# Kernel tuning notes

Hardware: AMD Instinct MI355X
Metric: run time of the kernel (lower is better)

The kernel has to match this reference:

```python
import jax, jax.numpy as jnp
import numpy as np

RES_SAMPLE = [-0.4, -0.3, -0.2, -0.1, 0.0, 0.1, 0.2, 0.3, 0.4]
GROUP_NUM = 8


def setup_inputs() -> dict:
    key = jax.random.key(0)
    k1, k2, k3, k4 = jax.random.split(key, 4)
    B, C, H, W = 4, 32, 256, 256
    return {
        "feat_ref": jax.random.normal(k1, (B, C, H, W), dtype=jnp.float32),
        "feat_ls": jax.random.normal(k2, (B, C, H, W), dtype=jnp.float32),
        "feat_rs": jax.random.normal(k3, (B, C, H, W), dtype=jnp.float32),
        "disp_init": jax.random.uniform(k4, (B, 1, H, W), dtype=jnp.float32),
    }


def _bilerp_chw(feat, x, y):
    """Bilinear sample feat [C,H,W] at pixel coords x,y [H,W], zeros padding
    (matches F.grid_sample(mode='bilinear', padding_mode='zeros'))."""
    C, H, W = feat.shape
    x0 = jnp.floor(x); y0 = jnp.floor(y)
    x1 = x0 + 1.0;     y1 = y0 + 1.0
    wx1 = x - x0; wx0 = 1.0 - wx1
    wy1 = y - y0; wy0 = 1.0 - wy1

    def gather(yi, xi):
        valid = (yi >= 0) & (yi <= H - 1) & (xi >= 0) & (xi <= W - 1)
        yc = jnp.clip(yi, 0, H - 1).astype(jnp.int32)
        xc = jnp.clip(xi, 0, W - 1).astype(jnp.int32)
        return feat[:, yc, xc] * valid.astype(feat.dtype)  # [C,H,W]

    return (gather(y0, x0) * (wy0 * wx0)
            + gather(y0, x1) * (wy0 * wx1)
            + gather(y1, x0) * (wy1 * wx0)
            + gather(y1, x1) * (wy1 * wx1))


def _warp_all_disp(feat, disp, x_dist):
    """feat [B,C,H,W], disp [B,D,H,W] -> warped [B,C,D,H,W] (y_dist=0)."""
    B, C, H, W = feat.shape
    xx = jnp.arange(W, dtype=feat.dtype)[None, :] * jnp.ones((H, 1), feat.dtype)  # [H,W]
    yy = jnp.arange(H, dtype=feat.dtype)[:, None] * jnp.ones((1, W), feat.dtype)  # [H,W]

    def per_b(feat_b, disp_b):  # feat_b [C,H,W], disp_b [D,H,W]
        x = xx[None] + x_dist * disp_b                      # [D,H,W]
        y = jnp.broadcast_to(yy, x.shape)                   # [D,H,W]
        return jax.vmap(lambda xs, ys: _bilerp_chw(feat_b, xs, ys))(x, y)  # [D,C,H,W]

    out = jax.vmap(per_b)(feat, disp)                       # [B,D,C,H,W]
    return out.transpose(0, 2, 1, 3, 4)                     # [B,C,D,H,W]


def reference(feat_ref, feat_ls, feat_rs, disp_init):
    B, C, H, W = feat_ref.shape
    res = jnp.asarray(RES_SAMPLE, dtype=feat_ref.dtype)     # [D]
    D = res.shape[0]
    disp = disp_init[:, 0][:, None] + res[None, :, None, None]  # [B,D,H,W]

    warp_left = _warp_all_disp(feat_ls, disp, 1.0)          # [B,C,D,H,W]
    warp_right = _warp_all_disp(feat_rs, disp, -1.0)        # [B,C,D,H,W]
    fr = feat_ref[:, :, None]                                # [B,C,1,H,W]

    mu = (warp_left + warp_right + fr) / 3.0
    var = ((warp_left - mu) ** 2 + (warp_right - mu) ** 2 + (fr - mu) ** 2) / 3.0

    cpg = C // GROUP_NUM
    cost = var.reshape(B, GROUP_NUM, cpg, D, H, W).mean(axis=2)  # [B,G,D,H,W]
    return cost
```

## Files before the change

kernel.cpp:

```cpp
#include <hip/hip_runtime.h>


#define B_ 4
#define C_ 32
#define H_ 256
#define W_ 256
#define D_ 9
#define G_ 8
#define CPG 4
#define HW_ (H_ * W_)
#define SW_ 260

typedef float v2f __attribute__((ext_vector_type(2)));

static __device__ __forceinline__ v2f sp(float x) {
    v2f r; r.x = x; r.y = x; return r;
}

__global__ __launch_bounds__(256) void cost_volume_kernel(
    const float* __restrict__ fref,
    const float* __restrict__ fls,
    const float* __restrict__ frs,
    const float* __restrict__ disp0,
    float* __restrict__ out)
{
    const float kRes[D_] = {-0.4f, -0.3f, -0.2f, -0.1f, 0.0f,
                             0.1f,  0.2f,  0.3f,  0.4f};

    __shared__ float sL[CPG][SW_];
    __shared__ float sR[CPG][SW_];

    const int bid = blockIdx.x;
    const int g = bid & (G_ - 1);
    const int t = bid >> 3;
    const int h = t & (H_ - 1);
    const int b = t >> 8;
    const int w = threadIdx.x;

    const float dbase = disp0[(unsigned)((b * H_ + h) * W_ + w)];

    const unsigned rowbase = (unsigned)(((b * C_ + g * CPG) * HW_) + h * W_);
    const float* __restrict__ refrow = fref + rowbase;
    const float* __restrict__ lsrow  = fls  + rowbase;
    const float* __restrict__ rsrow  = frs  + rowbase;

    {
        const int x = w - 2;
        const bool v = (unsigned)x < (unsigned)W_;
        #pragma unroll
        for (int cc = 0; cc < CPG; ++cc) {
            sL[cc][w] = v ? lsrow[cc * HW_ + x] : 0.0f;
            sR[cc][w] = v ? rsrow[cc * HW_ + x] : 0.0f;
        }
        if (w < SW_ - W_) {
            const int x2 = W_ - 2 + w;
            const bool v2 = x2 < W_;
            #pragma unroll
            for (int cc = 0; cc < CPG; ++cc) {
                sL[cc][W_ + w] = v2 ? lsrow[cc * HW_ + x2] : 0.0f;
                sR[cc][W_ + w] = v2 ? rsrow[cc * HW_ + x2] : 0.0f;
            }
        }
    }

    v2f fr01, fr23;
    fr01.x = refrow[(unsigned)w];
    fr01.y = refrow[HW_ + (unsigned)w];
    fr23.x = refrow[2u * HW_ + (unsigned)w];
    fr23.y = refrow[3u * HW_ + (unsigned)w];
    const float frq = fr01.x * fr01.x + fr01.y * fr01.y
                    + fr23.x * fr23.x + fr23.y * fr23.y;

    __syncthreads();

    const float wf = (float)w;
    const float s0 = wf + dbase;
    const int i0l = (int)floorf(s0 - 0.4f);
    int relL = i0l - w;
    relL = relL < -1 ? -1 : (relL > 0 ? 0 : relL);
    const float a1l = (s0 - (float)(w + relL)) - 1.0f;

    const float s1 = wf - dbase;
    const int i0r = (int)floorf(s1 - 0.4f);
    int relR = i0r - w;
    relR = relR < -2 ? -2 : (relR > -1 ? -1 : relR);
    const float a1r = (s1 - (float)(w + relR)) - 1.0f;

    const int baseL = w + relL + 2;
    const int baseR = w + relR + 2;

    v2f tl01[3], tl23[3], tr01[3], tr23[3];
    #pragma unroll
    for (int k = 0; k < 3; ++k) {
        tl01[k].x = sL[0][baseL + k];
        tl01[k].y = sL[1][baseL + k];
        tl23[k].x = sL[2][baseL + k];
        tl23[k].y = sL[3][baseL + k];
        tr01[k].x = sR[0][baseR + k];
        tr01[k].y = sR[1][baseR + k];
        tr23[k].x = sR[2][baseR + k];
        tr23[k].y = sR[3][baseR + k];
    }

    const unsigned obase = (unsigned)(((b * G_ + g) * D_) * HW_ + h * W_ + w);

    #pragma unroll
    for (int d = 0; d < D_; ++d) {
        const float tlw = a1l + kRes[d];
        const float W0l = fmaxf(-tlw, 0.0f);
        const float W1l = 1.0f - fabsf(tlw);
        const float W2l = fmaxf(tlw, 0.0f);
        const float trw = a1r - kRes[d];
        const float W0r = fmaxf(-trw, 0.0f);
        const float W1r = 1.0f - fabsf(trw);
        const float W2r = fmaxf(trw, 0.0f);

        v2f wl01 = tl01[0] * sp(W0l) + tl01[1] * sp(W1l) + tl01[2] * sp(W2l);
        v2f wl23 = tl23[0] * sp(W0l) + tl23[1] * sp(W1l) + tl23[2] * sp(W2l);
        v2f wr01 = tr01[0] * sp(W0r) + tr01[1] * sp(W1r) + tr01[2] * sp(W2r);
        v2f wr23 = tr23[0] * sp(W0r) + tr23[1] * sp(W1r) + tr23[2] * sp(W2r);

        v2f q   = wl01 * wl01 + wr01 * wr01 + wl23 * wl23 + wr23 * wr23;
        v2f s01 = wl01 + wr01 + fr01;
        v2f s23 = wl23 + wr23 + fr23;
        v2f s2  = s01 * s01 + s23 * s23;

        const float Q  = q.x + q.y + frq;
        const float S2 = s2.x + s2.y;
        const float val = (Q - S2 * (1.0f / 3.0f)) * (1.0f / 12.0f);
        __builtin_nontemporal_store(val, &out[obase + (unsigned)d * (unsigned)HW_]);
    }
}

extern "C" void kernel_launch(void* const* d_in, const int* in_sizes, int n_in,
                              void* d_out, int out_size, void* d_ws, size_t ws_size,
                              hipStream_t stream) {
    const float* fref  = (const float*)d_in[0];
    const float* fls   = (const float*)d_in[1];
    const float* frs   = (const float*)d_in[2];
    const float* disp0 = (const float*)d_in[3];
    float* out = (float*)d_out;

    dim3 grid(B_ * H_ * G_);
    dim3 block(W_);
    cost_volume_kernel<<<grid, block, 0, stream>>>(fref, fls, frs, disp0, out);
}
```

Measured before the change: 161.9 us.

## Process four rows per block with register-prefetched double-buffered shared rows

Each block now handles four consecutive image rows instead of one. While the current row is computed, the next row's left/right/ref features are prefetched into registers, then written into a second LDS buffer. The halo load is remapped onto 32 threads. This cuts the block count by 4x and aims to hide global load latency behind compute, at the cost of extra barriers per row and higher register pressure.

```diff
diff --git a/kernel.cpp b/kernel.cpp
--- a/kernel.cpp
+++ b/kernel.cpp
@@ -10,6 +10,7 @@
 #define CPG 4
 #define HW_ (H_ * W_)
 #define SW_ 260
+#define ROWS 4
 
 typedef float v2f __attribute__((ext_vector_type(2)));
 
@@ -27,108 +28,140 @@
     const float kRes[D_] = {-0.4f, -0.3f, -0.2f, -0.1f, 0.0f,
                              0.1f,  0.2f,  0.3f,  0.4f};
 
-    __shared__ float sL[CPG][SW_];
-    __shared__ float sR[CPG][SW_];
+    __shared__ float sL[2][CPG][SW_];
+    __shared__ float sR[2][CPG][SW_];
 
     const int bid = blockIdx.x;
-    const int g = bid & (G_ - 1);
-    const int t = bid >> 3;
-    const int h = t & (H_ - 1);
-    const int b = t >> 8;
-    const int w = threadIdx.x;
+    const int g  = bid & (G_ - 1);
+    const int t  = bid >> 3;
+    const int h0 = (t & (H_ / ROWS - 1)) * ROWS;
+    const int b  = t >> 6;
+    const int w  = threadIdx.x;
 
-    const float dbase = disp0[(unsigned)((b * H_ + h) * W_ + w)];
+    const unsigned dbbase = (unsigned)((b * H_ + h0) * W_ + w);
+    float dsp[ROWS];
+    #pragma unroll
+    for (int r = 0; r < ROWS; ++r) dsp[r] = disp0[dbbase + (unsigned)(r * W_)];
 
-    const unsigned rowbase = (unsigned)(((b * C_ + g * CPG) * HW_) + h * W_);
-    const float* __restrict__ refrow = fref + rowbase;
-    const float* __restrict__ lsrow  = fls  + rowbase;
-    const float* __restrict__ rsrow  = frs  + rowbase;
+    const unsigned rowbase0 = (unsigned)(((b * C_ + g * CPG) * HW_) + h0 * W_);
 
-    {
-        const int x = w - 2;
-        const bool v = (unsigned)x < (unsigned)W_;
+    float rL[CPG], rR[CPG], rF[CPG], hx = 0.0f;
+    const bool vmain = (w >= 2);
+    const int  xmain = w - 2;
+    const int hcs = w >> 2, hk = w & 3;
+    const int hx2 = 254 + hk;
+    const bool hval = (w < 32) && (hx2 < W_);
+
+    auto LOADROW = [&](int r) {
+        const float* __restrict__ ls = fls  + rowbase0 + (unsigned)(r * W_);
+        const float* __restrict__ rs = frs  + rowbase0 + (unsigned)(r * W_);
+        const float* __restrict__ rf = fref + rowbase0 + (unsigned)(r * W_);
         #pragma unroll
         for (int cc = 0; cc < CPG; ++cc) {
-            sL[cc][w] = v ? lsrow[cc * HW_ + x] : 0.0f;
-            sR[cc][w] = v ? rsrow[cc * HW_ + x] : 0.0f;
+            rL[cc] = vmain ? ls[cc * HW_ + xmain] : 0.0f;
+            rR[cc] = vmain ? rs[cc * HW_ + xmain] : 0.0f;
+            rF[cc] = rf[cc * HW_ + w];
         }
-        if (w < SW_ - W_) {
-            const int x2 = W_ - 2 + w;
-            const bool v2 = x2 < W_;
-            #pragma unroll
-            for (int cc = 0; cc < CPG; ++cc) {
-                sL[cc][W_ + w] = v2 ? lsrow[cc * HW_ + x2] : 0.0f;
-                sR[cc][W_ + w] = v2 ? rsrow[cc * HW_ + x2] : 0.0f;
-            }
+        if (w < 32) {
+            const float* p = (hcs < 4) ? ls : rs;
+            hx = hval ? p[(hcs & 3) * HW_ + hx2] : 0.0f;
         }
-    }
+    };
+    auto WRITEROW = [&](int buf) {
+        #pragma unroll
+        for (int cc = 0; cc < CPG; ++cc) {
+            sL[buf][cc][w] = rL[cc];
+            sR[buf][cc][w] = rR[cc];
+        }
+        if (w < 32) {
+            if (hcs < 4) sL[buf][hcs][256 + hk] = hx;
+            else         sR[buf][hcs & 3][256 + hk] = hx;
+        }
+    };
 
-    v2f fr01, fr23;
-    fr01.x = refrow[(unsigned)w];
-    fr01.y = refrow[HW_ + (unsigned)w];
-    fr23.x = refrow[2u * HW_ + (unsigned)w];
-    fr23.y = refrow[3u * HW_ + (unsigned)w];
-    const float frq = fr01.x * fr01.x + fr01.y * fr01.y
-                    + fr23.x * fr23.x + fr23.y * fr23.y;
-
+    LOADROW(0);
+    WRITEROW(0);
     __syncthreads();
 
     const float wf = (float)w;
-    const float s0 = wf + dbase;
-    const int i0l = (int)floorf(s0 - 0.4f);
-    int relL = i0l - w;
-    relL = relL < -1 ? -1 : (relL > 0 ? 0 : relL);
-    const float a1l = (s0 - (float)(w + relL)) - 1.0f;
-
-    const float s1 = wf - dbase;
-    const int i0r = (int)floorf(s1 - 0.4f);
-    int relR = i0r - w;
-    relR = relR < -2 ? -2 : (relR > -1 ? -1 : relR);
-    const float a1r = (s1 - (float)(w + relR)) - 1.0f;
-
-    const int baseL = w + relL + 2;
-    const int baseR = w + relR + 2;
-
-    v2f tl01[3], tl23[3], tr01[3], tr23[3];
-    #pragma unroll
-    for (int k = 0; k < 3; ++k) {
-        tl01[k].x = sL[0][baseL + k];
-        tl01[k].y = sL[1][baseL + k];
-        tl23[k].x = sL[2][baseL + k];
-        tl23[k].y = sL[3][baseL + k];
-        tr01[k].x = sR[0][baseR + k];
-        tr01[k].y = sR[1][baseR + k];
-        tr23[k].x = sR[2][baseR + k];
-        tr23[k].y = sR[3][baseR + k];
-    }
-
-    const unsigned obase = (unsigned)(((b * G_ + g) * D_) * HW_ + h * W_ + w);
+    int cur = 0;
 
     #pragma unroll
-    for (int d = 0; d < D_; ++d) {
-        const float tlw = a1l + kRes[d];
-        const float W0l = fmaxf(-tlw, 0.0f);
-        const float W1l = 1.0f - fabsf(tlw);
-        const float W2l = fmaxf(tlw, 0.0f);
-        const float trw = a1r - kRes[d];
-        const float W0r = fmaxf(-trw, 0.0f);
-        const float W1r = 1.0f - fabsf(trw);
-        const float W2r = fmaxf(trw, 0.0f);
+    for (int r = 0; r < ROWS; ++r) {
+        v2f fr01, fr23;
+        fr01.x = rF[0]; fr01.y = rF[1];
+        fr23.x = rF[2]; fr23.y = rF[3];
+        const float frq = fr01.x * fr01.x + fr01.y * fr01.y
+                        + fr23.x * fr23.x + fr23.y * fr23.y;
 
-        v2f wl01 = tl01[0] * sp(W0l) + tl01[1] * sp(W1l) + tl01[2] * sp(W2l);
-        v2f wl23 = tl23[0] * sp(W0l) + tl23[1] * sp(W1l) + tl23[2] * sp(W2l);
-        v2f wr01 = tr01[0] * sp(W0r) + tr01[1] * sp(W1r) + tr01[2] * sp(W2r);
-        v2f wr23 = tr23[0] * sp(W0r) + tr23[1] * sp(W1r) + tr23[2] * sp(W2r);
+        if (r + 1 < ROWS) LOADROW(r + 1);
 
-        v2f q   = wl01 * wl01 + wr01 * wr01 + wl23 * wl23 + wr23 * wr23;
-        v2f s01 = wl01 + wr01 + fr01;
-        v2f s23 = wl23 + wr23 + fr23;
-        v2f s2  = s01 * s01 + s23 * s23;
+        const float dbase = dsp[r];
+        const float s0 = wf + dbase;
+        const int i0l = (int)floorf(s0 - 0.4f);
+        int relL = i0l - w;
+        relL = relL < -1 ? -1 : (relL > 0 ? 0 : relL);
+        const float a1l = (s0 - (float)(w + relL)) - 1.0f;
 
-        const float Q  = q.x + q.y + frq;
-        const float S2 = s2.x + s2.y;
-        const float val = (Q - S2 * (1.0f / 3.0f)) * (1.0f / 12.0f);
-        __builtin_nontemporal_store(val, &out[obase + (unsigned)d * (unsigned)HW_]);
+        const float s1 = wf - dbase;
+        const int i0r = (int)floorf(s1 - 0.4f);
+        int relR = i0r - w;
+        relR = relR < -2 ? -2 : (relR > -1 ? -1 : relR);
+        const float a1r = (s1 - (float)(w + relR)) - 1.0f;
+
+        const int baseL = w + relL + 2;
+        const int baseR = w + relR + 2;
+
+        v2f tl01[3], tl23[3], tr01[3], tr23[3];
+        #pragma unroll
+        for (int k = 0; k < 3; ++k) {
+            tl01[k].x = sL[cur][0][baseL + k];
+            tl01[k].y = sL[cur][1][baseL + k];
+            tl23[k].x = sL[cur][2][baseL + k];
+            tl23[k].y = sL[cur][3][baseL + k];
+            tr01[k].x = sR[cur][0][baseR + k];
+            tr01[k].y = sR[cur][1][baseR + k];
+            tr23[k].x = sR[cur][2][baseR + k];
+            tr23[k].y = sR[cur][3][baseR + k];
+        }
+
+        const unsigned obase =
+            (unsigned)(((b * G_ + g) * D_) * HW_ + (h0 + r) * W_ + w);
+
+        #pragma unroll
+        for (int d = 0; d < D_; ++d) {
+            const float tlw = a1l + kRes[d];
+            const float W0l = fmaxf(-tlw, 0.0f);
+            const float W1l = 1.0f - fabsf(tlw);
+            const float W2l = fmaxf(tlw, 0.0f);
+            const float trw = a1r - kRes[d];
+            const float W0r = fmaxf(-trw, 0.0f);
+            const float W1r = 1.0f - fabsf(trw);
+            const float W2r = fmaxf(trw, 0.0f);
+
+            v2f wl01 = tl01[0] * sp(W0l) + tl01[1] * sp(W1l) + tl01[2] * sp(W2l);
+            v2f wl23 = tl23[0] * sp(W0l) + tl23[1] * sp(W1l) + tl23[2] * sp(W2l);
+            v2f wr01 = tr01[0] * sp(W0r) + tr01[1] * sp(W1r) + tr01[2] * sp(W2r);
+            v2f wr23 = tr23[0] * sp(W0r) + tr23[1] * sp(W1r) + tr23[2] * sp(W2r);
+
+            v2f q   = wl01 * wl01 + wr01 * wr01 + wl23 * wl23 + wr23 * wr23;
+            v2f s01 = wl01 + wr01 + fr01;
+            v2f s23 = wl23 + wr23 + fr23;
+            v2f s2  = s01 * s01 + s23 * s23;
+
+            const float Q  = q.x + q.y + frq;
+            const float S2 = s2.x + s2.y;
+            const float val = (Q - S2 * (1.0f / 3.0f)) * (1.0f / 12.0f);
+            __builtin_nontemporal_store(
+                val, &out[obase + (unsigned)d * (unsigned)HW_]);
+        }
+
+        if (r + 1 < ROWS) {
+            __syncthreads();
+            WRITEROW(cur ^ 1);
+            __syncthreads();
+            cur ^= 1;
+        }
     }
 }
 
@@ -141,7 +174,7 @@
     const float* disp0 = (const float*)d_in[3];
     float* out = (float*)d_out;
 
-    dim3 grid(B_ * H_ * G_);
+    dim3 grid(B_ * G_ * (H_ / ROWS));
     dim3 block(W_);
     cost_volume_kernel<<<grid, block, 0, stream>>>(fref, fls, frs, disp0, out);
 }
```

After: 163.8 us. Within noise of the previous version (+1.1%).

## Process eight rows per block and defer output stores until after a cooperative grid sync

Applied to the files above, without the earlier changes.

Each block now handles eight image rows instead of one, shrinking the grid to 1024 blocks with launch bounds requesting four blocks per CU. It launches cooperatively, keeps all 72 outputs per thread in registers, and stores them only after a grid-wide sync, apparently to separate the read phase from the write phase across the whole GPU. If the cooperative launch fails, it falls back to a normal launch that stores each value as it is computed. Risks include heavy register pressure from the stash, the cost of the grid barrier, and fewer blocks in flight to hide latency.

```diff
diff --git a/kernel.cpp b/kernel.cpp
--- a/kernel.cpp
+++ b/kernel.cpp
@@ -1,4 +1,5 @@
 #include <hip/hip_runtime.h>
+#include <hip/hip_cooperative_groups.h>
 
 
 #define B_ 4
@@ -10,14 +11,16 @@
 #define CPG 4
 #define HW_ (H_ * W_)
 #define SW_ 260
+#define ROWS 8
+
+namespace cg = cooperative_groups;
 
 typedef float v2f __attribute__((ext_vector_type(2)));
 
-static __device__ __forceinline__ v2f sp(float x) {
-    v2f r; r.x = x; r.y = x; return r;
-}
+static __device__ __forceinline__ v2f sp(float x) { v2f r; r.x = x; r.y = x; return r; }
 
-__global__ __launch_bounds__(256) void cost_volume_kernel(
+template <bool COOP>
+__global__ __launch_bounds__(256, 4) void cost_volume_kernel(
     const float* __restrict__ fref,
     const float* __restrict__ fls,
     const float* __restrict__ frs,
@@ -31,104 +34,131 @@
     __shared__ float sR[CPG][SW_];
 
     const int bid = blockIdx.x;
-    const int g = bid & (G_ - 1);
-    const int t = bid >> 3;
-    const int h = t & (H_ - 1);
-    const int b = t >> 8;
-    const int w = threadIdx.x;
+    const int g  = bid & (G_ - 1);
+    const int t  = bid >> 3;
+    const int b  = t >> 5;
+    const int h0 = (t & 31) * ROWS;
+    const int w  = threadIdx.x;
+    const float wf = (float)w;
 
-    const float dbase = disp0[(unsigned)((b * H_ + h) * W_ + w)];
+    float stash[ROWS][D_];
 
-    const unsigned rowbase = (unsigned)(((b * C_ + g * CPG) * HW_) + h * W_);
-    const float* __restrict__ refrow = fref + rowbase;
-    const float* __restrict__ lsrow  = fls  + rowbase;
-    const float* __restrict__ rsrow  = frs  + rowbase;
+    const unsigned rowbase0 = (unsigned)(((b * C_ + g * CPG) * HW_) + h0 * W_);
+    const unsigned obase0 = (unsigned)(((b * G_ + g) * D_) * HW_ + h0 * W_ + w);
 
-    {
-        const int x = w - 2;
-        const bool v = (unsigned)x < (unsigned)W_;
-        #pragma unroll
-        for (int cc = 0; cc < CPG; ++cc) {
-            sL[cc][w] = v ? lsrow[cc * HW_ + x] : 0.0f;
-            sR[cc][w] = v ? rsrow[cc * HW_ + x] : 0.0f;
-        }
-        if (w < SW_ - W_) {
-            const int x2 = W_ - 2 + w;
-            const bool v2 = x2 < W_;
+    #pragma unroll
+    for (int r = 0; r < ROWS; ++r) {
+        const int h = h0 + r;
+        const float dbase = disp0[(unsigned)((b * H_ + h) * W_ + w)];
+
+        const float* __restrict__ lsrow = fls  + rowbase0 + (unsigned)(r * W_);
+        const float* __restrict__ rsrow = frs  + rowbase0 + (unsigned)(r * W_);
+        const float* __restrict__ rfrow = fref + rowbase0 + (unsigned)(r * W_);
+
+        {
+            const int x = w - 2;
+            const bool v = (unsigned)x < (unsigned)W_;
             #pragma unroll
             for (int cc = 0; cc < CPG; ++cc) {
-                sL[cc][W_ + w] = v2 ? lsrow[cc * HW_ + x2] : 0.0f;
-                sR[cc][W_ + w] = v2 ? rsrow[cc * HW_ + x2] : 0.0f;
+                sL[cc][w] = v ? lsrow[cc * HW_ + x] : 0.0f;
+                sR[cc][w] = v ? rsrow[cc * HW_ + x] : 0.0f;
+            }
+            if (w < SW_ - W_) {
+                const int x2 = W_ - 2 + w;
+                const bool v2 = x2 < W_;
+                #pragma unroll
+                for (int cc = 0; cc < CPG; ++cc) {
+                    sL[cc][W_ + w] = v2 ? lsrow[cc * HW_ + x2] : 0.0f;
+                    sR[cc][W_ + w] = v2 ? rsrow[cc * HW_ + x2] : 0.0f;
+                }
             }
         }
+
+        v2f fr01, fr23;
+        fr01.x = rfrow[(unsigned)w];
+        fr01.y = rfrow[HW_ + (unsigned)w];
+        fr23.x = rfrow[2u * HW_ + (unsigned)w];
+        fr23.y = rfrow[3u * HW_ + (unsigned)w];
+        const float frq = fr01.x * fr01.x + fr01.y * fr01.y
+                        + fr23.x * fr23.x + fr23.y * fr23.y;
+
+        __syncthreads();
+
+        const float s0 = wf + dbase;
+        const int i0l = (int)floorf(s0 - 0.4f);
+        int relL = i0l - w;
+        relL = relL < -1 ? -1 : (relL > 0 ? 0 : relL);
+        const float a1l = (s0 - (float)(w + relL)) - 1.0f;
+
+        const float s1 = wf - dbase;
+        const int i0r = (int)floorf(s1 - 0.4f);
+        int relR = i0r - w;
+        relR = relR < -2 ? -2 : (relR > -1 ? -1 : relR);
+        const float a1r = (s1 - (float)(w + relR)) - 1.0f;
+
+        const int baseL = w + relL + 2;
+        const int baseR = w + relR + 2;
+
+        v2f tl01[3], tl23[3], tr01[3], tr23[3];
+        #pragma unroll
+        for (int k = 0; k < 3; ++k) {
+            tl01[k].x = sL[0][baseL + k];
+            tl01[k].y = sL[1][baseL + k];
+            tl23[k].x = sL[2][baseL + k];
+            tl23[k].y = sL[3][baseL + k];
+            tr01[k].x = sR[0][baseR + k];
+            tr01[k].y = sR[1][baseR + k];
+            tr23[k].x = sR[2][baseR + k];
+            tr23[k].y = sR[3][baseR + k];
+        }
+
+        #pragma unroll
+        for (int d = 0; d < D_; ++d) {
+            const float tlw = a1l + kRes[d];
+            const float W0l = fmaxf(-tlw, 0.0f);
+            const float W1l = 1.0f - fabsf(tlw);
+            const float W2l = fmaxf(tlw, 0.0f);
+            const float trw = a1r - kRes[d];
+            const float W0r = fmaxf(-trw, 0.0f);
+            const float W1r = 1.0f - fabsf(trw);
+            const float W2r = fmaxf(trw, 0.0f);
+
+            v2f wl01 = tl01[0] * sp(W0l) + tl01[1] * sp(W1l) + tl01[2] * sp(W2l);
+            v2f wl23 = tl23[0] * sp(W0l) + tl23[1] * sp(W1l) + tl23[2] * sp(W2l);
+            v2f wr01 = tr01[0] * sp(W0r) + tr01[1] * sp(W1r) + tr01[2] * sp(W2r);
+            v2f wr23 = tr23[0] * sp(W0r) + tr23[1] * sp(W1r) + tr23[2] * sp(W2r);
+
+            v2f q   = wl01 * wl01 + wr01 * wr01 + wl23 * wl23 + wr23 * wr23;
+            v2f s01 = wl01 + wr01 + fr01;
+            v2f s23 = wl23 + wr23 + fr23;
+            v2f s2  = s01 * s01 + s23 * s23;
+
+            const float Q  = q.x + q.y + frq;
+            const float S2 = s2.x + s2.y;
+            const float val = (Q - S2 * (1.0f / 3.0f)) * (1.0f / 12.0f);
+
+            if constexpr (COOP) {
+                stash[r][d] = val;
+            } else {
+                __builtin_nontemporal_store(
+                    val, &out[obase0 + (unsigned)(d * HW_ + r * W_)]);
+            }
+        }
+
+        if (r + 1 < ROWS) __syncthreads();
     }
 
-    v2f fr01, fr23;
-    fr01.x = refrow[(unsigned)w];
-    fr01.y = refrow[HW_ + (unsigned)w];
-    fr23.x = refrow[2u * HW_ + (unsigned)w];
-    fr23.y = refrow[3u * HW_ + (unsigned)w];
-    const float frq = fr01.x * fr01.x + fr01.y * fr01.y
-                    + fr23.x * fr23.x + fr23.y * fr23.y;
+    if constexpr (COOP) {
+        cg::this_grid().sync();
 
-    __syncthreads();
-
-    const float wf = (float)w;
-    const float s0 = wf + dbase;
-    const int i0l = (int)floorf(s0 - 0.4f);
-    int relL = i0l - w;
-    relL = relL < -1 ? -1 : (relL > 0 ? 0 : relL);
-    const float a1l = (s0 - (float)(w + relL)) - 1.0f;
-
-    const float s1 = wf - dbase;
-    const int i0r = (int)floorf(s1 - 0.4f);
-    int relR = i0r - w;
-    relR = relR < -2 ? -2 : (relR > -1 ? -1 : relR);
-    const float a1r = (s1 - (float)(w + relR)) - 1.0f;
-
-    const int baseL = w + relL + 2;
-    const int baseR = w + relR + 2;
-
-    v2f tl01[3], tl23[3], tr01[3], tr23[3];
-    #pragma unroll
-    for (int k = 0; k < 3; ++k) {
-        tl01[k].x = sL[0][baseL + k];
-        tl01[k].y = sL[1][baseL + k];
-        tl23[k].x = sL[2][baseL + k];
-        tl23[k].y = sL[3][baseL + k];
-        tr01[k].x = sR[0][baseR + k];
-        tr01[k].y = sR[1][baseR + k];
-        tr23[k].x = sR[2][baseR + k];
-        tr23[k].y = sR[3][baseR + k];
-    }
-
-    const unsigned obase = (unsigned)(((b * G_ + g) * D_) * HW_ + h * W_ + w);
-
-    #pragma unroll
-    for (int d = 0; d < D_; ++d) {
-        const float tlw = a1l + kRes[d];
-        const float W0l = fmaxf(-tlw, 0.0f);
-        const float W1l = 1.0f - fabsf(tlw);
-        const float W2l = fmaxf(tlw, 0.0f);
-        const float trw = a1r - kRes[d];
-        const float W0r = fmaxf(-trw, 0.0f);
-        const float W1r = 1.0f - fabsf(trw);
-        const float W2r = fmaxf(trw, 0.0f);
-
-        v2f wl01 = tl01[0] * sp(W0l) + tl01[1] * sp(W1l) + tl01[2] * sp(W2l);
-        v2f wl23 = tl23[0] * sp(W0l) + tl23[1] * sp(W1l) + tl23[2] * sp(W2l);
-        v2f wr01 = tr01[0] * sp(W0r) + tr01[1] * sp(W1r) + tr01[2] * sp(W2r);
-        v2f wr23 = tr23[0] * sp(W0r) + tr23[1] * sp(W1r) + tr23[2] * sp(W2r);
-
-        v2f q   = wl01 * wl01 + wr01 * wr01 + wl23 * wl23 + wr23 * wr23;
-        v2f s01 = wl01 + wr01 + fr01;
-        v2f s23 = wl23 + wr23 + fr23;
-        v2f s2  = s01 * s01 + s23 * s23;
-
-        const float Q  = q.x + q.y + frq;
-        const float S2 = s2.x + s2.y;
-        const float val = (Q - S2 * (1.0f / 3.0f)) * (1.0f / 12.0f);
-        __builtin_nontemporal_store(val, &out[obase + (unsigned)d * (unsigned)HW_]);
+        #pragma unroll
+        for (int d = 0; d < D_; ++d) {
+            #pragma unroll
+            for (int r = 0; r < ROWS; ++r) {
+                __builtin_nontemporal_store(
+                    stash[r][d] , &out[obase0 + (unsigned)(d * HW_ + r * W_)]);
+            }
+        }
     }
 }
 
@@ -141,7 +171,15 @@
     const float* disp0 = (const float*)d_in[3];
     float* out = (float*)d_out;
 
-    dim3 grid(B_ * H_ * G_);
-    dim3 block(W_);
-    cost_volume_kernel<<<grid, block, 0, stream>>>(fref, fls, frs, disp0, out);
+    dim3 grid(B_ * G_ * (H_ / ROWS));
+    dim3 block(256);
+
+    void* args[] = {(void*)&fref, (void*)&fls, (void*)&frs,
+                    (void*)&disp0, (void*)&out};
+    hipError_t e = hipLaunchCooperativeKernel(
+        (const void*)&cost_volume_kernel<true>, grid, block, args, 0, stream);
+    if (e != hipSuccess) {
+        cost_volume_kernel<false><<<grid, block, 0, stream>>>(
+            fref, fls, frs, disp0, out);
+    }
 }
```

Measured after the change: 368.2 us. 2.27x slower.

## Process two pixels per thread with vectorized loads/stores and reorder block mapping

Applied to the files above, without the earlier changes.

Each thread now handles two adjacent pixels, which halves the block to 128 threads and allows 8-byte vector loads of features, disparity and reference and 8-byte nontemporal stores of the output. The block index is remapped so that consecutive blocks walk rows h within the same (b,g), and the shared-memory halo fill is restructured around the padded row width. This is meant to cut memory instruction count and improve coalescing, at the cost of more registers per thread and fewer threads in flight.

```diff
diff --git a/kernel.cpp b/kernel.cpp
--- a/kernel.cpp
+++ b/kernel.cpp
@@ -9,15 +9,13 @@
 #define G_ 8
 #define CPG 4
 #define HW_ (H_ * W_)
-#define SW_ 260
+#define SWPAD 264
 
 typedef float v2f __attribute__((ext_vector_type(2)));
 
-static __device__ __forceinline__ v2f sp(float x) {
-    v2f r; r.x = x; r.y = x; return r;
-}
+static __device__ __forceinline__ v2f sp(float x) { v2f r; r.x = x; r.y = x; return r; }
 
-__global__ __launch_bounds__(256) void cost_volume_kernel(
+__global__ __launch_bounds__(128) void cost_volume_kernel(
     const float* __restrict__ fref,
     const float* __restrict__ fls,
     const float* __restrict__ frs,
@@ -27,17 +25,17 @@
     const float kRes[D_] = {-0.4f, -0.3f, -0.2f, -0.1f, 0.0f,
                              0.1f,  0.2f,  0.3f,  0.4f};
 
-    __shared__ float sL[CPG][SW_];
-    __shared__ float sR[CPG][SW_];
+    __shared__ float sL[CPG][SWPAD];
+    __shared__ float sR[CPG][SWPAD];
 
     const int bid = blockIdx.x;
-    const int g = bid & (G_ - 1);
-    const int t = bid >> 3;
-    const int h = t & (H_ - 1);
-    const int b = t >> 8;
-    const int w = threadIdx.x;
+    const int h = bid & (H_ - 1);
+    const int b = (bid >> 8) & (B_ - 1);
+    const int g = bid >> 10;
+    const int t = threadIdx.x;
+    const int w0 = t << 1;
 
-    const float dbase = disp0[(unsigned)((b * H_ + h) * W_ + w)];
+    const v2f dsp = *(const v2f*)(disp0 + (unsigned)((b * H_ + h) * W_ + w0));
 
     const unsigned rowbase = (unsigned)(((b * C_ + g * CPG) * HW_) + h * W_);
     const float* __restrict__ refrow = fref + rowbase;
@@ -45,90 +43,112 @@
     const float* __restrict__ rsrow  = frs  + rowbase;
 
     {
-        const int x = w - 2;
-        const bool v = (unsigned)x < (unsigned)W_;
+        const int x0 = w0 - 2;
+        const bool v = (x0 >= 0);
         #pragma unroll
         for (int cc = 0; cc < CPG; ++cc) {
-            sL[cc][w] = v ? lsrow[cc * HW_ + x] : 0.0f;
-            sR[cc][w] = v ? rsrow[cc * HW_ + x] : 0.0f;
+            v2f mv = v ? *(const v2f*)(lsrow + cc * HW_ + x0) : sp(0.0f);
+            *(v2f*)&sL[cc][w0] = mv;
+            v2f mr = v ? *(const v2f*)(rsrow + cc * HW_ + x0) : sp(0.0f);
+            *(v2f*)&sR[cc][w0] = mr;
         }
-        if (w < SW_ - W_) {
-            const int x2 = W_ - 2 + w;
-            const bool v2 = x2 < W_;
-            #pragma unroll
-            for (int cc = 0; cc < CPG; ++cc) {
-                sL[cc][W_ + w] = v2 ? lsrow[cc * HW_ + x2] : 0.0f;
-                sR[cc][W_ + w] = v2 ? rsrow[cc * HW_ + x2] : 0.0f;
+        if (t < 16) {
+            const int side = t >> 3;
+            const int cc   = (t >> 1) & 3;
+            const int part = t & 1;
+            v2f hv = sp(0.0f);
+            if (part == 0) {
+                const float* src = (side ? rsrow : lsrow) + cc * HW_ + 254;
+                hv = *(const v2f*)src;
             }
+            float* dst = side ? &sR[cc][256 + 2 * part] : &sL[cc][256 + 2 * part];
+            *(v2f*)dst = hv;
         }
     }
 
-    v2f fr01, fr23;
-    fr01.x = refrow[(unsigned)w];
-    fr01.y = refrow[HW_ + (unsigned)w];
-    fr23.x = refrow[2u * HW_ + (unsigned)w];
-    fr23.y = refrow[3u * HW_ + (unsigned)w];
-    const float frq = fr01.x * fr01.x + fr01.y * fr01.y
-                    + fr23.x * fr23.x + fr23.y * fr23.y;
+    v2f F[CPG];
+    #pragma unroll
+    for (int cc = 0; cc < CPG; ++cc)
+        F[cc] = *(const v2f*)(refrow + cc * HW_ + w0);
 
     __syncthreads();
 
-    const float wf = (float)w;
-    const float s0 = wf + dbase;
-    const int i0l = (int)floorf(s0 - 0.4f);
-    int relL = i0l - w;
-    relL = relL < -1 ? -1 : (relL > 0 ? 0 : relL);
-    const float a1l = (s0 - (float)(w + relL)) - 1.0f;
-
-    const float s1 = wf - dbase;
-    const int i0r = (int)floorf(s1 - 0.4f);
-    int relR = i0r - w;
-    relR = relR < -2 ? -2 : (relR > -1 ? -1 : relR);
-    const float a1r = (s1 - (float)(w + relR)) - 1.0f;
-
-    const int baseL = w + relL + 2;
-    const int baseR = w + relR + 2;
-
-    v2f tl01[3], tl23[3], tr01[3], tr23[3];
-    #pragma unroll
-    for (int k = 0; k < 3; ++k) {
-        tl01[k].x = sL[0][baseL + k];
-        tl01[k].y = sL[1][baseL + k];
-        tl23[k].x = sL[2][baseL + k];
-        tl23[k].y = sL[3][baseL + k];
-        tr01[k].x = sR[0][baseR + k];
-        tr01[k].y = sR[1][baseR + k];
-        tr23[k].x = sR[2][baseR + k];
-        tr23[k].y = sR[3][baseR + k];
-    }
-
-    const unsigned obase = (unsigned)(((b * G_ + g) * D_) * HW_ + h * W_ + w);
+    const unsigned obase = (unsigned)(((b * G_ + g) * D_) * HW_ + h * W_ + w0);
+    float vals0[D_];
 
     #pragma unroll
-    for (int d = 0; d < D_; ++d) {
-        const float tlw = a1l + kRes[d];
-        const float W0l = fmaxf(-tlw, 0.0f);
-        const float W1l = 1.0f - fabsf(tlw);
-        const float W2l = fmaxf(tlw, 0.0f);
-        const float trw = a1r - kRes[d];
-        const float W0r = fmaxf(-trw, 0.0f);
-        const float W1r = 1.0f - fabsf(trw);
-        const float W2r = fmaxf(trw, 0.0f);
+    for (int p = 0; p < 2; ++p) {
+        const int w = w0 + p;
+        const float wf = (float)w;
+        const float dbase = p ? dsp.y : dsp.x;
 
-        v2f wl01 = tl01[0] * sp(W0l) + tl01[1] * sp(W1l) + tl01[2] * sp(W2l);
-        v2f wl23 = tl23[0] * sp(W0l) + tl23[1] * sp(W1l) + tl23[2] * sp(W2l);
-        v2f wr01 = tr01[0] * sp(W0r) + tr01[1] * sp(W1r) + tr01[2] * sp(W2r);
-        v2f wr23 = tr23[0] * sp(W0r) + tr23[1] * sp(W1r) + tr23[2] * sp(W2r);
+        const float s0 = wf + dbase;
+        const int i0l = (int)floorf(s0 - 0.4f);
+        int relL = i0l - w;
+        relL = relL < -1 ? -1 : (relL > 0 ? 0 : relL);
+        const float a1l = (s0 - (float)(w + relL)) - 1.0f;
 
-        v2f q   = wl01 * wl01 + wr01 * wr01 + wl23 * wl23 + wr23 * wr23;
-        v2f s01 = wl01 + wr01 + fr01;
-        v2f s23 = wl23 + wr23 + fr23;
-        v2f s2  = s01 * s01 + s23 * s23;
+        const float s1 = wf - dbase;
+        const int i0r = (int)floorf(s1 - 0.4f);
+        int relR = i0r - w;
+        relR = relR < -2 ? -2 : (relR > -1 ? -1 : relR);
+        const float a1r = (s1 - (float)(w + relR)) - 1.0f;
 
-        const float Q  = q.x + q.y + frq;
-        const float S2 = s2.x + s2.y;
-        const float val = (Q - S2 * (1.0f / 3.0f)) * (1.0f / 12.0f);
-        __builtin_nontemporal_store(val, &out[obase + (unsigned)d * (unsigned)HW_]);
+        const int baseL = w + relL + 2;
+        const int baseR = w + relR + 2;
+
+        v2f fr01, fr23;
+        fr01.x = p ? F[0].y : F[0].x;  fr01.y = p ? F[1].y : F[1].x;
+        fr23.x = p ? F[2].y : F[2].x;  fr23.y = p ? F[3].y : F[3].x;
+        const float frq = fr01.x * fr01.x + fr01.y * fr01.y
+                        + fr23.x * fr23.x + fr23.y * fr23.y;
+
+        v2f tl01[3], tl23[3], tr01[3], tr23[3];
+        #pragma unroll
+        for (int k = 0; k < 3; ++k) {
+            tl01[k].x = sL[0][baseL + k];
+            tl01[k].y = sL[1][baseL + k];
+            tl23[k].x = sL[2][baseL + k];
+            tl23[k].y = sL[3][baseL + k];
+            tr01[k].x = sR[0][baseR + k];
+            tr01[k].y = sR[1][baseR + k];
+            tr23[k].x = sR[2][baseR + k];
+            tr23[k].y = sR[3][baseR + k];
+        }
+
+        #pragma unroll
+        for (int d = 0; d < D_; ++d) {
+            const float tlw = a1l + kRes[d];
+            const float W0l = fmaxf(-tlw, 0.0f);
+            const float W1l = 1.0f - fabsf(tlw);
+            const float W2l = fmaxf(tlw, 0.0f);
+            const float trw = a1r - kRes[d];
+            const float W0r = fmaxf(-trw, 0.0f);
+            const float W1r = 1.0f - fabsf(trw);
+            const float W2r = fmaxf(trw, 0.0f);
+
+            v2f wl01 = tl01[0] * sp(W0l) + tl01[1] * sp(W1l) + tl01[2] * sp(W2l);
+            v2f wl23 = tl23[0] * sp(W0l) + tl23[1] * sp(W1l) + tl23[2] * sp(W2l);
+            v2f wr01 = tr01[0] * sp(W0r) + tr01[1] * sp(W1r) + tr01[2] * sp(W2r);
+            v2f wr23 = tr23[0] * sp(W0r) + tr23[1] * sp(W1r) + tr23[2] * sp(W2r);
+
+            v2f q   = wl01 * wl01 + wr01 * wr01 + wl23 * wl23 + wr23 * wr23;
+            v2f s01 = wl01 + wr01 + fr01;
+            v2f s23 = wl23 + wr23 + fr23;
+            v2f s2  = s01 * s01 + s23 * s23;
+
+            const float Q  = q.x + q.y + frq;
+            const float S2 = s2.x + s2.y;
+            const float val = (Q - S2 * (1.0f / 3.0f)) * (1.0f / 12.0f);
+
+            if (p == 0) {
+                vals0[d] = val;
+            } else {
+                v2f o; o.x = vals0[d]; o.y = val;
+                __builtin_nontemporal_store(
+                    o, (v2f*)(out + obase + (unsigned)d * (unsigned)HW_));
+            }
+        }
     }
 }
 
@@ -141,7 +161,7 @@
     const float* disp0 = (const float*)d_in[3];
     float* out = (float*)d_out;
 
-    dim3 grid(B_ * H_ * G_);
-    dim3 block(W_);
+    dim3 grid(B_ * G_ * H_);
+    dim3 block(128);
     cost_volume_kernel<<<grid, block, 0, stream>>>(fref, fls, frs, disp0, out);
 }
```

Result: no change. 162.5 us (+0.4%).
